# Performance work log

Measured on AMD Instinct MI355X. Metric: run time of the kernel, lower is better.

The kernel has to match this reference:

```python
import jax, jax.numpy as jnp
import numpy as np

N, M, D0, D1, H, E = 1024, 4096, 1024, 512, 512, 64
TAU = 0.5


def setup_inputs() -> dict:
    key = jax.random.key(0)
    ks = jax.random.split(key, 24)
    g = lambda k, shape, s=0.05: (jax.random.normal(k, shape, jnp.float32) * s)
    # 0/1 meta-path neighbor incidence matrices, avg degree ~16
    nei0 = (jax.random.uniform(ks[0], (N, M)) < 0.004).astype(jnp.float32)
    nei1 = (jax.random.uniform(ks[1], (N, M)) < 0.004).astype(jnp.float32)
    def norm_adj(k):
        a = (jax.random.uniform(k, (N, N)) < 0.005).astype(jnp.float32) + jnp.eye(N, dtype=jnp.float32)
        return a / a.sum(1, keepdims=True)
    return dict(
        feat0=g(ks[2], (N, D0), 1.0), feat1=g(ks[3], (M, D1), 1.0), feat2=g(ks[4], (M, D1), 1.0),
        mask_feat=g(ks[5], (N, D0), 1.0),
        nei0=nei0, nei1=nei1,
        adj0=norm_adj(ks[6]), adj1=norm_adj(ks[7]),
        madj0=norm_adj(ks[8]), madj1=norm_adj(ks[9]),
        fc0_w=g(ks[10], (D0, H)), fc0_b=jnp.zeros((H,), jnp.float32),
        fc1_w=g(ks[11], (D1, H)), fc1_b=jnp.zeros((H,), jnp.float32),
        fc2_w=g(ks[12], (D1, H)), fc2_b=jnp.zeros((H,), jnp.float32),
        agg0_w=g(ks[13], (H, H)), agg1_w=g(ks[14], (H, H)),
        gcn_w1=g(ks[15], (H, E)), gcn_b1=jnp.zeros((E,), jnp.float32),
        gcn_w2=g(ks[16], (E, E)), gcn_b2=jnp.zeros((E,), jnp.float32),
        att_w=g(ks[17], (E, E)), att_b=jnp.zeros((E,), jnp.float32),
        att_vec=g(ks[18], (E,)),
        proj_w=g(ks[19], (E, E)), proj_b=jnp.zeros((E,), jnp.float32),
        mlp1_w=g(ks[20], (E, 16)), mlp1_b=jnp.zeros((16,), jnp.float32),
        mlp2_w=g(ks[21], (16, 1)), mlp2_b=jnp.zeros((1,), jnp.float32),
    )


def _l2norm(x):
    # F.normalize(dim=1)
    return x / jnp.maximum(jnp.linalg.norm(x, axis=1, keepdims=True), 1e-12)


def reference(feat0, feat1, feat2, mask_feat, nei0, nei1, adj0, adj1, madj0, madj1,
              fc0_w, fc0_b, fc1_w, fc1_b, fc2_w, fc2_b, agg0_w, agg1_w,
              gcn_w1, gcn_b1, gcn_w2, gcn_b2, att_w, att_b, att_vec,
              proj_w, proj_b, mlp1_w, mlp1_b, mlp2_w, mlp2_b):
    elu = jax.nn.elu
    # aggregate_nei_acm (dropout in eval mode => identity)
    h_tar = elu(feat0 @ fc0_w + fc0_b)                       # [N, H]
    h_mask = elu(mask_feat @ fc0_w + fc0_b)                  # [N, H]
    h_nei = [elu(feat1 @ fc1_w + fc1_b), elu(feat2 @ fc2_w + fc2_b)]  # [M, H]
    neis = [nei0, nei1]
    agg_ws = [agg0_w, agg1_w]
    views, masks = [], []
    for i in range(2):
        cnt = jnp.maximum(neis[i].sum(1, keepdims=True), 1.0)  # nei_index_count, clamped >0
        h_agg = (neis[i] @ h_nei[i]) / cnt                     # sparse neighbor mean, [N, H]
        t = h_agg @ agg_ws[i]
        views.append(elu(h_tar + t))
        masks.append(elu(h_mask + t))

    def gcn(x, adj):
        # 2-layer GCN: relu(A X W1 + b1) -> A H W2 + b2
        h = jax.nn.relu(adj @ (x @ gcn_w1) + gcn_b1)
        return adj @ (h @ gcn_w2) + gcn_b2

    mean_adj = (adj0 + adj1) * 0.5                           # torch.stack(adjs).mean(0)
    z_coarse = gcn(h_tar, mean_adj)                          # [N, E]
    # order: Encoder(view_i, adj_i), Encoder(mask_i, mask_adj_i) per i
    h_fine = [gcn(views[0], adj0), gcn(masks[0], madj0),
              gcn(views[1], adj1), gcn(masks[1], madj1)]
    hs = jnp.stack([_l2norm(h) for h in h_fine])             # [V=4, N, E]
    # semantic attention over views
    e = jnp.einsum('vne,e->v', jnp.tanh(hs @ att_w + att_b), att_vec) / hs.shape[1]
    beta = jax.nn.softmax(e)
    z_fine = jnp.einsum('v,vne->ne', beta, hs)               # [N, E]
    zc = _l2norm(jnp.tanh(z_coarse @ proj_w + proj_b))
    zf = _l2norm(jnp.tanh(z_fine @ proj_w + proj_b))
    # weight_InfoNce
    logits = (zf @ zc.T) / TAU                               # [N, N]
    dots = jnp.exp(logits)
    pair = zf[:, None, :] + zc[None, :, :]                   # [N, N, E] = z_anchor[i] + z[j]
    w = jax.nn.sigmoid(jnp.tanh(pair @ mlp1_w + mlp1_b) @ mlp2_w + mlp2_b)[..., 0]
    denom = jnp.sum(dots * w, axis=1)
    # -log(diag(dots)/denom) = log(denom) - diag(logits)
    loss = jnp.mean(jnp.log(denom) - jnp.diagonal(logits))
    return loss
```

## Files before the change

kernel.cpp:

```cpp
#include <hip/hip_runtime.h>

#define ACT_NONE 0
#define ACT_ELU  1
#define ACT_RELU 2
#define ACT_TANH 3

typedef __attribute__((ext_vector_type(8))) short short8;
typedef __attribute__((ext_vector_type(4))) float f32x4;

__device__ __forceinline__ float frcp(float x) { return __builtin_amdgcn_rcpf(x); }
__device__ __forceinline__ float fexp(float x) { return __expf(x); }
__device__ __forceinline__ float ftanh(float x) {
    return 1.f - 2.f * frcp(fexp(2.f * x) + 1.f);
}
__device__ __forceinline__ float fsigmoid(float x) {
    return frcp(1.f + fexp(-x));
}

__device__ __forceinline__ float apply_act(float v, int act) {
    if (act == ACT_ELU)  return v > 0.f ? v : fexp(v) - 1.f;
    if (act == ACT_RELU) return fmaxf(v, 0.f);
    if (act == ACT_TANH) return ftanh(v);
    return v;
}

__device__ __forceinline__ unsigned short f2bf(float f) {
    unsigned int u = __float_as_uint(f);
    unsigned int r = (u + 0x7fffu + ((u >> 16) & 1u)) >> 16;
    return (unsigned short)r;
}
__device__ __forceinline__ float bf2f(unsigned short u) {
    return __uint_as_float(((unsigned int)u) << 16);
}

__device__ __forceinline__ void xcd_remap(int& bx, int& by, int nx, int ny) {
    if ((ny & 7) == 0) {
        int L = by * nx + bx;
        int xcd = L & 7, j = L >> 3;
        int q = j / nx;
        by = xcd + 8 * q;
        bx = j - q * nx;
    }
}

struct CTDesc { const float* in; unsigned short* out; int R, C, tcols, tile0; };
struct CMDesc { const float* in; unsigned short* out; int start4; };
struct CastArr {
    CTDesc t[8]; int nt; int T;
    CMDesc f[6]; int nf; int total4;
};

__global__ __launch_bounds__(256) void cast_all_kernel(CastArr a) {
    int b = blockIdx.x;
    if (b < a.T) {
        int s = 0;
        while (s + 1 < a.nt && b >= a.t[s + 1].tile0) ++s;
        const CTDesc d = a.t[s];
        int lt = b - d.tile0;
        int tr = lt / d.tcols, tc = lt % d.tcols;
        int r0 = tr * 32, c0 = tc * 32;
        __shared__ float tt[32][33];
        int tx = threadIdx.x & 31, ty = threadIdx.x >> 5;
        for (int i = ty; i < 32; i += 8) {
            int r = r0 + i, c = c0 + tx;
            tt[i][tx] = (r < d.R && c < d.C) ? d.in[(size_t)r * d.C + c] : 0.f;
        }
        __syncthreads();
        for (int i = ty; i < 32; i += 8) {
            int c = c0 + i, r = r0 + tx;
            if (c < d.C && r < d.R) d.out[(size_t)c * d.R + r] = f2bf(tt[tx][i]);
        }
    } else {
        int g4 = (b - a.T) * 256 + threadIdx.x;
        if (g4 >= a.total4) return;
        int s = 0;
        while (s + 1 < a.nf && g4 >= a.f[s + 1].start4) ++s;
        int l4 = g4 - a.f[s].start4;
        float4 v = *reinterpret_cast<const float4*>(a.f[s].in + (size_t)l4 * 4);
        ushort4 o;
        o.x = f2bf(v.x); o.y = f2bf(v.y); o.z = f2bf(v.z); o.w = f2bf(v.w);
        *reinterpret_cast<ushort4*>(a.f[s].out + (size_t)l4 * 4) = o;
    }
}

struct GSeg {
    const unsigned short* A;
    const unsigned short* Bt;
    const unsigned short* Bt2;
    const float* bias;
    const float* bias2;
    float* C;
    unsigned short* Cbf;
    unsigned short* Cbf2;
    int cbf_mlimit;
    int m_split;
    int K;
    int act;
    int mt0;
};
struct GArr { GSeg s[2]; int ns; int N; };

struct KBufs { short8 a0, a1, b0, b1; };

__global__ __launch_bounds__(256) void gemm_seg_kernel(GArr g) {
    int bx = blockIdx.x, by = blockIdx.y;
    xcd_remap(bx, by, gridDim.x, gridDim.y);
    const int mt = by;
    const int si = (g.ns > 1 && mt >= g.s[1].mt0) ? 1 : 0;
    const GSeg s = g.s[si];
    const int K = s.K, N = g.N;
    const int tid = threadIdx.x;
    const int w = tid >> 6, lane = tid & 63;
    const int wr = w >> 1, wc = w & 1;
    const int lr = lane & 15, lk = lane >> 4;
    const int bm = (mt - s.mt0) * 64, bn = bx * 64;
    const unsigned short* Bu = s.Bt;
    const float* bu = s.bias;
    if (bm >= s.m_split) { Bu = s.Bt2; bu = s.bias2; }

    const unsigned short* Ap = s.A + (size_t)(bm + wr * 32 + lr) * K + lk * 8;
    const unsigned short* Bp = Bu + (size_t)(bn + wc * 32 + lr) * K + lk * 8;
    const size_t r16A = (size_t)16 * K;

    f32x4 acc[2][2] = {};
    KBufs u0, u1, u2, u3;
    auto LD = [&](KBufs& u, int kk) {
        kk = kk < K ? kk : 0;
        u.a0 = *reinterpret_cast<const short8*>(Ap + kk);
        u.a1 = *reinterpret_cast<const short8*>(Ap + r16A + kk);
        u.b0 = *reinterpret_cast<const short8*>(Bp + kk);
        u.b1 = *reinterpret_cast<const short8*>(Bp + r16A + kk);
    };
    auto MM = [&](const KBufs& u) {
        acc[0][0] = __builtin_amdgcn_mfma_f32_16x16x32_bf16(u.a0, u.b0, acc[0][0], 0, 0, 0);
        acc[0][1] = __builtin_amdgcn_mfma_f32_16x16x32_bf16(u.a0, u.b1, acc[0][1], 0, 0, 0);
        acc[1][0] = __builtin_amdgcn_mfma_f32_16x16x32_bf16(u.a1, u.b0, acc[1][0], 0, 0, 0);
        acc[1][1] = __builtin_amdgcn_mfma_f32_16x16x32_bf16(u.a1, u.b1, acc[1][1], 0, 0, 0);
    };
    LD(u0, 0); LD(u1, 32); LD(u2, 64);
    for (int k = 0; k < K; k += 128) {
        LD(u3, k + 96);  MM(u0);
        LD(u0, k + 128); MM(u1);
        LD(u1, k + 160); MM(u2);
        LD(u2, k + 192); MM(u3);
    }
    #pragma unroll
    for (int i = 0; i < 2; ++i) {
        #pragma unroll
        for (int j = 0; j < 2; ++j) {
            int gcol = bn + wc * 32 + j * 16 + lr;
            float bv = bu ? bu[gcol] : 0.f;
            #pragma unroll
            for (int r = 0; r < 4; ++r) {
                int grow = bm + wr * 32 + i * 16 + lk * 4 + r;
                float v = apply_act(acc[i][j][r] + bv, s.act);
                if (s.C) s.C[(size_t)grow * N + gcol] = v;
                if (grow < s.cbf_mlimit) {
                    if (s.Cbf)  s.Cbf[(size_t)grow * N + gcol] = f2bf(v);
                } else {
                    if (s.Cbf2) s.Cbf2[(size_t)(grow - s.cbf_mlimit) * N + gcol] = f2bf(v);
                }
            }
        }
    }
}

__global__ __launch_bounds__(256) void gemm_splitk_kernel(
    const unsigned short* __restrict__ A, const unsigned short* __restrict__ Bt,
    const unsigned short* __restrict__ Bt2, int m_split,
    float* __restrict__ C, int M, int K, int N, int ksplit) {
    int bx = blockIdx.x, by = blockIdx.y;
    xcd_remap(bx, by, gridDim.x, gridDim.y);
    const int tid = threadIdx.x;
    const int w = tid >> 6, lane = tid & 63;
    const int wr = w >> 1, wc = w & 1;
    const int lr = lane & 15, lk = lane >> 4;
    const int bm = by * 64, bn = bx * 64;
    const int z = blockIdx.z;
    const int kbeg = z * ksplit;
    const int kend = kbeg + ksplit < K ? kbeg + ksplit : K;
    const int KL = kend - kbeg;
    C += (size_t)z * M * N;
    const unsigned short* Bu = (bm >= m_split) ? Bt2 : Bt;

    const unsigned short* Ap = A + (size_t)(bm + wr * 32 + lr) * K + kbeg + lk * 8;
    const unsigned short* Bp = Bu + (size_t)(bn + wc * 32 + lr) * K + kbeg + lk * 8;
    const size_t r16 = (size_t)16 * K;

    f32x4 acc[2][2] = {};
    KBufs u0, u1, u2, u3;
    auto LD = [&](KBufs& u, int kk) {
        kk = kk < KL ? kk : 0;
        u.a0 = *reinterpret_cast<const short8*>(Ap + kk);
        u.a1 = *reinterpret_cast<const short8*>(Ap + r16 + kk);
        u.b0 = *reinterpret_cast<const short8*>(Bp + kk);
        u.b1 = *reinterpret_cast<const short8*>(Bp + r16 + kk);
    };
    auto MM = [&](const KBufs& u) {
        acc[0][0] = __builtin_amdgcn_mfma_f32_16x16x32_bf16(u.a0, u.b0, acc[0][0], 0, 0, 0);
        acc[0][1] = __builtin_amdgcn_mfma_f32_16x16x32_bf16(u.a0, u.b1, acc[0][1], 0, 0, 0);
        acc[1][0] = __builtin_amdgcn_mfma_f32_16x16x32_bf16(u.a1, u.b0, acc[1][0], 0, 0, 0);
        acc[1][1] = __builtin_amdgcn_mfma_f32_16x16x32_bf16(u.a1, u.b1, acc[1][1], 0, 0, 0);
    };
    LD(u0, 0); LD(u1, 32); LD(u2, 64);
    for (int k = 0; k < KL; k += 128) {
        LD(u3, k + 96);  MM(u0);
        LD(u0, k + 128); MM(u1);
        LD(u1, k + 160); MM(u2);
        LD(u2, k + 192); MM(u3);
    }
    #pragma unroll
    for (int i = 0; i < 2; ++i)
        #pragma unroll
        for (int j = 0; j < 2; ++j) {
            int gcol = bn + wc * 32 + j * 16 + lr;
            #pragma unroll
            for (int r = 0; r < 4; ++r) {
                int grow = bm + wr * 32 + i * 16 + lk * 4 + r;
                C[(size_t)grow * N + gcol] = acc[i][j][r];
            }
        }
}

__global__ __launch_bounds__(256) void neiagg_kernel(
    const float* __restrict__ nei0, const float* __restrict__ nei1,
    const unsigned short* __restrict__ hn0, const unsigned short* __restrict__ hn1,
    unsigned short* __restrict__ hagg) {
    const int row = blockIdx.x, br = blockIdx.y, t = threadIdx.x;
    const float* nei = br ? nei1 : nei0;
    const unsigned short* hn = br ? hn1 : hn0;
    __shared__ int idxs[256];
    __shared__ int cnt;
    if (t == 0) cnt = 0;
    __syncthreads();
    const float4* nr = reinterpret_cast<const float4*>(nei + (size_t)row * 4096);
    for (int j = t; j < 1024; j += 256) {
        float4 v = nr[j];
        if (v.x != 0.f) { int s = atomicAdd(&cnt, 1); if (s < 256) idxs[s] = j * 4 + 0; }
        if (v.y != 0.f) { int s = atomicAdd(&cnt, 1); if (s < 256) idxs[s] = j * 4 + 1; }
        if (v.z != 0.f) { int s = atomicAdd(&cnt, 1); if (s < 256) idxs[s] = j * 4 + 2; }
        if (v.w != 0.f) { int s = atomicAdd(&cnt, 1); if (s < 256) idxs[s] = j * 4 + 3; }
    }
    __syncthreads();
    int n = cnt < 256 ? cnt : 256;
    float inv = frcp(fmaxf((float)cnt, 1.f));
    int c = t * 2;
    float a0 = 0.f, a1 = 0.f, b0 = 0.f, b1 = 0.f;
    int k = 0;
    for (; k + 2 <= n; k += 2) {
        ushort2 u = *reinterpret_cast<const ushort2*>(&hn[(size_t)idxs[k] * 512 + c]);
        ushort2 v = *reinterpret_cast<const ushort2*>(&hn[(size_t)idxs[k + 1] * 512 + c]);
        a0 += bf2f(u.x); a1 += bf2f(u.y);
        b0 += bf2f(v.x); b1 += bf2f(v.y);
    }
    if (k < n) {
        ushort2 u = *reinterpret_cast<const ushort2*>(&hn[(size_t)idxs[k] * 512 + c]);
        a0 += bf2f(u.x); a1 += bf2f(u.y);
    }
    ushort2 o; o.x = f2bf((a0 + b0) * inv); o.y = f2bf((a1 + b1) * inv);
    *reinterpret_cast<ushort2*>(&hagg[((size_t)br * 1024 + row) * 512 + c]) = o;
}

__global__ void addelu_kernel(const unsigned short* __restrict__ ht,
                              const unsigned short* __restrict__ hm,
                              const float* __restrict__ tt, unsigned short* __restrict__ xcat,
                              int nh, int PL) {
    int idx = blockIdx.x * 256 + threadIdx.x;
    if (idx < nh) {
        float h1 = bf2f(ht[idx]), h2 = bf2f(hm[idx]);
        float t0 = tt[idx] + tt[idx + PL];
        float t1 = tt[idx + nh] + tt[idx + nh + PL];
        float a = h1 + t0, b = h2 + t0, c = h1 + t1, d = h2 + t1;
        xcat[(size_t)1 * nh + idx] = f2bf(a > 0.f ? a : fexp(a) - 1.f);
        xcat[(size_t)2 * nh + idx] = f2bf(b > 0.f ? b : fexp(b) - 1.f);
        xcat[(size_t)3 * nh + idx] = f2bf(c > 0.f ? c : fexp(c) - 1.f);
        xcat[(size_t)4 * nh + idx] = f2bf(d > 0.f ? d : fexp(d) - 1.f);
    }
}

__global__ __launch_bounds__(64) void adjprep_kernel(
    const float* __restrict__ adj0, const float* __restrict__ adj1,
    const float* __restrict__ madj0, const float* __restrict__ madj1,
    int* __restrict__ cnts, int* __restrict__ idxs, float* __restrict__ wts) {
    const int row = blockIdx.x, br = blockIdx.y, t = threadIdx.x;
    const float* Aa; const float* Ab = nullptr; float sc = 1.f;
    if (br == 0)      { Aa = adj0; Ab = adj1; sc = 0.5f; }
    else if (br == 1) { Aa = adj0; }
    else if (br == 2) { Aa = madj0; }
    else if (br == 3) { Aa = adj1; }
    else              { Aa = madj1; }
    __shared__ int li[128];
    __shared__ float lw[128];
    __shared__ int cnt;
    if (t == 0) cnt = 0;
    __syncthreads();
    const float4* ar = reinterpret_cast<const float4*>(Aa + (size_t)row * 1024);
    const float4* brp = Ab ? reinterpret_cast<const float4*>(Ab + (size_t)row * 1024) : nullptr;
    for (int j = t; j < 256; j += 64) {
        float4 v = ar[j];
        if (brp) { float4 u = brp[j]; v.x += u.x; v.y += u.y; v.z += u.z; v.w += u.w; }
        if (v.x != 0.f) { int s = atomicAdd(&cnt, 1); if (s < 128) { li[s] = j * 4 + 0; lw[s] = v.x * sc; } }
        if (v.y != 0.f) { int s = atomicAdd(&cnt, 1); if (s < 128) { li[s] = j * 4 + 1; lw[s] = v.y * sc; } }
        if (v.z != 0.f) { int s = atomicAdd(&cnt, 1); if (s < 128) { li[s] = j * 4 + 2; lw[s] = v.z * sc; } }
        if (v.w != 0.f) { int s = atomicAdd(&cnt, 1); if (s < 128) { li[s] = j * 4 + 3; lw[s] = v.w * sc; } }
    }
    __syncthreads();
    int n = cnt < 128 ? cnt : 128;
    size_t base = ((size_t)br * 1024 + row) * 128;
    for (int k = t; k < n; k += 64) { idxs[base + k] = li[k]; wts[base + k] = lw[k]; }
    if (t == 0) cnts[br * 1024 + row] = n;
}

__global__ __launch_bounds__(256) void spmm1_kernel(
    const int* __restrict__ cnts, const int* __restrict__ idxs, const float* __restrict__ wts,
    const float* __restrict__ X, int PL, const float* __restrict__ bias,
    unsigned short* __restrict__ out) {
    const int row = blockIdx.x * 4 + (threadIdx.x >> 6);
    const int br = blockIdx.y, t = threadIdx.x & 63;
    size_t base = ((size_t)br * 1024 + row) * 128;
    int n = cnts[br * 1024 + row];
    const float* Xb = X + (size_t)br * 1024 * 64;
    const float* Xb2 = Xb + PL;
    float acc = bias[t], a1 = 0.f;
    int k = 0;
    for (; k + 2 <= n; k += 2) {
        int   i0 = idxs[base + k], i1 = idxs[base + k + 1];
        float w0 = wts[base + k],  w1 = wts[base + k + 1];
        acc += w0 * (Xb[(size_t)i0 * 64 + t] + Xb2[(size_t)i0 * 64 + t]);
        a1  += w1 * (Xb[(size_t)i1 * 64 + t] + Xb2[(size_t)i1 * 64 + t]);
    }
    if (k < n) {
        int i0 = idxs[base + k];
        acc += wts[base + k] * (Xb[(size_t)i0 * 64 + t] + Xb2[(size_t)i0 * 64 + t]);
    }
    acc += a1;
    out[((size_t)br * 1024 + row) * 64 + t] = f2bf(fmaxf(acc, 0.f));
}

__global__ __launch_bounds__(256) void spmm2_kernel(
    const int* __restrict__ cnts, const int* __restrict__ idxs, const float* __restrict__ wts,
    const unsigned short* __restrict__ H1, const float* __restrict__ w2,
    const float* __restrict__ b2, unsigned short* __restrict__ zcf_bf,
    float* __restrict__ hs, const float* __restrict__ att_w,
    const float* __restrict__ att_b, const float* __restrict__ att_vec,
    float* __restrict__ att_row) {
    const int wv = threadIdx.x >> 6;
    const int row = blockIdx.x * 4 + wv;
    const int br = blockIdx.y, t = threadIdx.x & 63;
    size_t base = ((size_t)br * 1024 + row) * 128;
    int n = cnts[br * 1024 + row];
    const unsigned short* Hb = H1 + (size_t)br * 1024 * 64;
    float g0 = 0.f, g1 = 0.f, g2 = 0.f, g3 = 0.f;
    int k = 0;
    for (; k + 4 <= n; k += 4) {
        g0 += wts[base + k]     * bf2f(Hb[(size_t)idxs[base + k]     * 64 + t]);
        g1 += wts[base + k + 1] * bf2f(Hb[(size_t)idxs[base + k + 1] * 64 + t]);
        g2 += wts[base + k + 2] * bf2f(Hb[(size_t)idxs[base + k + 2] * 64 + t]);
        g3 += wts[base + k + 3] * bf2f(Hb[(size_t)idxs[base + k + 3] * 64 + t]);
    }
    for (; k < n; ++k) g0 += wts[base + k] * bf2f(Hb[(size_t)idxs[base + k] * 64 + t]);
    float g = (g0 + g1) + (g2 + g3);
    __shared__ float rs[4][64];
    rs[wv][t] = g;
    float o = b2[t];
    #pragma unroll
    for (int c = 0; c < 64; ++c) o += rs[wv][c] * w2[c * 64 + t];
    if (br == 0) {
        zcf_bf[(size_t)row * 64 + t] = f2bf(o);
        return;
    }
    float s = o * o;
    #pragma unroll
    for (int q = 32; q; q >>= 1) s += __shfl_down(s, q);
    s = __shfl(s, 0);
    float v = o * frcp(fmaxf(sqrtf(s), 1e-12f));
    hs[((size_t)(br - 1) * 1024 + row) * 64 + t] = v;
    rs[wv][t] = v;
    float sa = att_b[t];
    #pragma unroll
    for (int c = 0; c < 64; ++c) sa += rs[wv][c] * att_w[c * 64 + t];
    float val = ftanh(sa) * att_vec[t];
    #pragma unroll
    for (int q = 32; q; q >>= 1) val += __shfl_down(val, q);
    if (t == 0) att_row[(size_t)(br - 1) * 1024 + row] = val;
}

__global__ __launch_bounds__(256) void attreduce_kernel(const float* __restrict__ att_row,
                                                        float* __restrict__ small) {
    const int v = blockIdx.x, t = threadIdx.x;
    const float* p = att_row + (size_t)v * 1024;
    float s = p[t] + p[t + 256] + p[t + 512] + p[t + 768];
    #pragma unroll
    for (int o = 32; o; o >>= 1) s += __shfl_down(s, o);
    __shared__ float ps[4];
    if ((t & 63) == 0) ps[t >> 6] = s;
    __syncthreads();
    if (t == 0) small[v] = ps[0] + ps[1] + ps[2] + ps[3];
}

__global__ __launch_bounds__(256) void projhead_kernel(
    const unsigned short* __restrict__ zcf_bf, const float* __restrict__ hs,
    const float* __restrict__ small, const float* __restrict__ proj_w,
    const float* __restrict__ proj_b, const float* __restrict__ mlp1_w,
    float* __restrict__ zcat, float* __restrict__ AC1) {
    const int wv = threadIdx.x >> 6;
    const int row = blockIdx.x * 4 + wv;
    const int t = threadIdx.x & 63;
    float zv;
    if (row < 1024) {
        zv = bf2f(zcf_bf[(size_t)row * 64 + t]);
    } else {
        int r = row - 1024;
        float e0 = small[0] * (1.f / 1024.f), e1 = small[1] * (1.f / 1024.f);
        float e2 = small[2] * (1.f / 1024.f), e3 = small[3] * (1.f / 1024.f);
        float mx = fmaxf(fmaxf(e0, e1), fmaxf(e2, e3));
        float x0 = expf(e0 - mx), x1 = expf(e1 - mx), x2 = expf(e2 - mx), x3 = expf(e3 - mx);
        float inv = 1.f / (x0 + x1 + x2 + x3);
        size_t ix = (size_t)r * 64 + t;
        zv = (x0 * hs[ix] + x1 * hs[ix + 65536] +
              x2 * hs[ix + 131072] + x3 * hs[ix + 196608]) * inv;
    }
    __shared__ float rs[4][64];
    rs[wv][t] = zv;
    float p = proj_b[t];
    #pragma unroll
    for (int c = 0; c < 64; ++c) p += rs[wv][c] * proj_w[c * 64 + t];
    p = ftanh(p);
    float s = p * p;
    #pragma unroll
    for (int q = 32; q; q >>= 1) s += __shfl_down(s, q);
    s = __shfl(s, 0);
    float r = p * frcp(fmaxf(sqrtf(s), 1e-12f));
    zcat[(size_t)row * 64 + t] = r;
    rs[wv][t] = r;
    if (t < 16) {
        float a = 0.f;
        #pragma unroll
        for (int c = 0; c < 64; ++c) a += rs[wv][c] * mlp1_w[c * 16 + t];
        AC1[(size_t)row * 16 + t] = a;
    }
}

__global__ __launch_bounds__(256) void infonce_kernel(
    const float* __restrict__ zf, const float* __restrict__ zc,
    const float* __restrict__ A1, const float* __restrict__ C1,
    const float* __restrict__ b1, const float* __restrict__ m2,
    const float* __restrict__ b2v, float* __restrict__ loss_acc) {
    const int i0 = blockIdx.x * 4, t = threadIdx.x;
    __shared__ __align__(16) float zfs[4][64];
    __shared__ float a1b[4][16], m2s[16];
    __shared__ float diag[4];
    __shared__ float wsum[4][4];
    if (t < 64) {
        #pragma unroll
        for (int ii = 0; ii < 4; ++ii) zfs[ii][t] = zf[(size_t)(i0 + ii) * 64 + t];
    }
    if (t < 16) {
        float bb = b1[t];
        #pragma unroll
        for (int ii = 0; ii < 4; ++ii) a1b[ii][t] = A1[(size_t)(i0 + ii) * 16 + t] + bb;
        m2s[t] = m2[t];
    }
    __syncthreads();
    const float b2 = b2v[0];
    float acc[4] = {};
    for (int j = t; j < 1024; j += 256) {
        const float4* zcj = reinterpret_cast<const float4*>(zc + (size_t)j * 64);
        float dot[4] = {};
        #pragma unroll
        for (int e = 0; e < 16; ++e) {
            float4 b = zcj[e];
            #pragma unroll
            for (int ii = 0; ii < 4; ++ii) {
                float4 a = reinterpret_cast<const float4*>(zfs[ii])[e];
                dot[ii] += a.x * b.x + a.y * b.y + a.z * b.z + a.w * b.w;
            }
        }
        float c1j[16];
        #pragma unroll
        for (int q = 0; q < 4; ++q) {
            float4 c4 = reinterpret_cast<const float4*>(C1 + (size_t)j * 16)[q];
            c1j[q * 4 + 0] = c4.x; c1j[q * 4 + 1] = c4.y;
            c1j[q * 4 + 2] = c4.z; c1j[q * 4 + 3] = c4.w;
        }
        #pragma unroll
        for (int ii = 0; ii < 4; ++ii) {
            float logit = dot[ii] * 2.0f;
            float h = b2;
            #pragma unroll
            for (int k = 0; k < 16; ++k) h += ftanh(a1b[ii][k] + c1j[k]) * m2s[k];
            acc[ii] += fexp(logit) * fsigmoid(h);
            if (j == i0 + ii) diag[ii] = logit;
        }
    }
    #pragma unroll
    for (int ii = 0; ii < 4; ++ii) {
        float a = acc[ii];
        #pragma unroll
        for (int o = 32; o; o >>= 1) a += __shfl_down(a, o);
        if ((t & 63) == 0) wsum[t >> 6][ii] = a;
    }
    __syncthreads();
    if (t == 0) {
        float part = 0.f;
        #pragma unroll
        for (int ii = 0; ii < 4; ++ii) {
            float denom = wsum[0][ii] + wsum[1][ii] + wsum[2][ii] + wsum[3][ii];
            part += logf(denom) - diag[ii];
        }
        atomicAdd(loss_acc, part);
    }
}

__global__ void finalize_kernel(const float* __restrict__ small, float* __restrict__ out) {
    if (threadIdx.x == 0) out[0] = small[4] * (1.f / 1024.f);
}

extern "C" void kernel_launch(void* const* d_in, const int* in_sizes, int n_in,
                              void* d_out, int out_size, void* d_ws, size_t ws_size,
                              hipStream_t stream) {
    const float* feat0     = (const float*)d_in[0];
    const float* feat1     = (const float*)d_in[1];
    const float* feat2     = (const float*)d_in[2];
    const float* mask_feat = (const float*)d_in[3];
    const float* nei0      = (const float*)d_in[4];
    const float* nei1      = (const float*)d_in[5];
    const float* adj0      = (const float*)d_in[6];
    const float* adj1      = (const float*)d_in[7];
    const float* madj0     = (const float*)d_in[8];
    const float* madj1     = (const float*)d_in[9];
    const float* fc0_w = (const float*)d_in[10];
    const float* fc0_b = (const float*)d_in[11];
    const float* fc1_w = (const float*)d_in[12];
    const float* fc1_b = (const float*)d_in[13];
    const float* fc2_w = (const float*)d_in[14];
    const float* fc2_b = (const float*)d_in[15];
    const float* agg0_w = (const float*)d_in[16];
    const float* agg1_w = (const float*)d_in[17];
    const float* gcn_w1 = (const float*)d_in[18];
    const float* gcn_b1 = (const float*)d_in[19];
    const float* gcn_w2 = (const float*)d_in[20];
    const float* gcn_b2 = (const float*)d_in[21];
    const float* att_w  = (const float*)d_in[22];
    const float* att_b  = (const float*)d_in[23];
    const float* att_vec = (const float*)d_in[24];
    const float* proj_w = (const float*)d_in[25];
    const float* proj_b = (const float*)d_in[26];
    const float* mlp1_w = (const float*)d_in[27];
    const float* mlp1_b = (const float*)d_in[28];
    const float* mlp2_w = (const float*)d_in[29];
    const float* mlp2_b = (const float*)d_in[30];

    const int N = 1024, M = 4096, D0 = 1024, D1 = 512, H = 512, E = 64;
    typedef unsigned short bf;

    float* W = (float*)d_ws;
    size_t off = 0;
    auto allocf = [&](size_t n) { float* p = W + off; off += n; return p; };
    float* tbuf    = allocf((size_t)2 * 2 * N * H);
    float* xw1cat  = allocf((size_t)2 * 5 * N * E);
    float* hs      = allocf((size_t)4 * N * E);
    float* zcat    = allocf((size_t)2 * N * E);
    float* AC1     = allocf((size_t)2 * N * 16);
    float* att_row = allocf((size_t)4 * N);
    float* small   = allocf(16);
    float* adj_wts = allocf((size_t)5 * 1024 * 128);
    int*   adj_idx = (int*)allocf((size_t)5 * 1024 * 128);
    int*   adj_cnt = (int*)allocf((size_t)5 * 1024);
    bf* BP = (bf*)(W + off);
    size_t boff = 0;
    auto allocb = [&](size_t n) { bf* p = BP + boff; boff += n; return p; };
    bf* feat0_bf = allocb((size_t)N * D0);
    bf* mask_bf  = allocb((size_t)N * D0);
    bf* feat1_bf = allocb((size_t)M * D1);
    bf* feat2_bf = allocb((size_t)M * D1);
    bf* xcat_bf  = allocb((size_t)5 * N * H);
    bf* hmask_bf = allocb((size_t)N * H);
    bf* hnei0_bf = allocb((size_t)M * H);
    bf* hnei1_bf = allocb((size_t)M * H);
    bf* hagg_bf  = allocb((size_t)2 * N * H);
    bf* h1cat_bf = allocb((size_t)5 * N * E);
    bf* zcf_bf   = allocb((size_t)N * E);
    bf* fc0_wT  = allocb((size_t)H * D0);
    bf* fc1_wT  = allocb((size_t)H * D1);
    bf* fc2_wT  = allocb((size_t)H * D1);
    bf* agg0_wT = allocb((size_t)H * H);
    bf* agg1_wT = allocb((size_t)H * H);
    bf* gw1_T   = allocb((size_t)E * H);

    hipMemsetAsync((void*)small, 0, 16 * sizeof(float), stream);

    {
        CastArr a; int tile = 0, i = 0;
        auto addT = [&](const float* in, bf* out, int R, int C) {
            int tc = (C + 31) / 32, trn = (R + 31) / 32;
            a.t[i++] = CTDesc{in, out, R, C, tc, tile};
            tile += tc * trn;
        };
        addT(fc0_w, fc0_wT, D0, H);
        addT(fc1_w, fc1_wT, D1, H);
        addT(fc2_w, fc2_wT, D1, H);
        addT(agg0_w, agg0_wT, H, H);
        addT(agg1_w, agg1_wT, H, H);
        addT(gcn_w1, gw1_T, H, E);
        a.nt = i; a.T = tile;
        int s4 = 0, fi = 0;
        auto addF = [&](const float* in, bf* out, int n) {
            a.f[fi++] = CMDesc{in, out, s4}; s4 += n / 4;
        };
        addF(feat0, feat0_bf, N * D0);
        addF(mask_feat, mask_bf, N * D0);
        addF(feat1, feat1_bf, M * D1);
        addF(feat2, feat2_bf, M * D1);
        a.nf = fi; a.total4 = s4;
        int nb = tile + (s4 + 255) / 256;
        cast_all_kernel<<<nb, 256, 0, stream>>>(a);
    }
    adjprep_kernel<<<dim3(N, 5), 64, 0, stream>>>(adj0, adj1, madj0, madj1,
                                                  adj_cnt, adj_idx, adj_wts);

    {
        GArr g;
        g.s[0] = GSeg{feat0_bf, fc0_wT, nullptr, fc0_b, nullptr,
                      nullptr, xcat_bf, hmask_bf, N, 1 << 30, D0, ACT_ELU, 0};
        g.s[1] = GSeg{feat1_bf, fc1_wT, fc2_wT, fc1_b, fc2_b,
                      nullptr, hnei0_bf, nullptr, 2 * M, M, D1, ACT_ELU, 32};
        g.ns = 2; g.N = H;
        gemm_seg_kernel<<<dim3(H / 64, 32 + 128), 256, 0, stream>>>(g);
    }

    neiagg_kernel<<<dim3(N, 2), 256, 0, stream>>>(nei0, nei1, hnei0_bf, hnei1_bf, hagg_bf);
    gemm_splitk_kernel<<<dim3(H / 64, 2 * N / 64, 2), 256, 0, stream>>>(
        hagg_bf, agg0_wT, agg1_wT, N, tbuf, 2 * N, H, H, 256);
    addelu_kernel<<<(N * H + 255) / 256, 256, 0, stream>>>(xcat_bf, hmask_bf, tbuf, xcat_bf,
                                                           N * H, 2 * N * H);

    gemm_splitk_kernel<<<dim3(1, 5 * N / 64, 2), 256, 0, stream>>>(
        xcat_bf, gw1_T, nullptr, 1 << 30, xw1cat, 5 * N, H, E, 256);
    spmm1_kernel<<<dim3(N / 4, 5), 256, 0, stream>>>(adj_cnt, adj_idx, adj_wts,
                                                     xw1cat, 5 * N * E, gcn_b1, h1cat_bf);
    spmm2_kernel<<<dim3(N / 4, 5), 256, 0, stream>>>(adj_cnt, adj_idx, adj_wts, h1cat_bf,
                                                     gcn_w2, gcn_b2, zcf_bf, hs,
                                                     att_w, att_b, att_vec, att_row);
    attreduce_kernel<<<4, 256, 0, stream>>>(att_row, small);

    projhead_kernel<<<2 * N / 4, 256, 0, stream>>>(zcf_bf, hs, small, proj_w, proj_b,
                                                   mlp1_w, zcat, AC1);

    const float* zc = zcat;
    const float* zf = zcat + (size_t)N * E;
    const float* C1 = AC1;
    const float* A1 = AC1 + (size_t)N * 16;
    infonce_kernel<<<N / 4, 256, 0, stream>>>(zf, zc, A1, C1, mlp1_b, mlp2_w, mlp2_b, small + 4);

    finalize_kernel<<<1, 64, 0, stream>>>(small, (float*)d_out);
}
```

Baseline: 292.3 us.

## Use LDS-staged 128x128 GEMM tiles, fold adjprep into cast kernel, drop atomics

The segmented GEMM now uses 128x128 block tiles and stages A and B through shared memory with global_load_lds, so each wave reuses the staged fragments across a 4x4 MFMA grid instead of loading its own fragments from global memory. The adjacency-to-sparse preprocessing is merged into the cast kernel as extra blocks, which removes one launch. The loss reduction now writes per-block partials and sums them in the finalize kernel, which removes the memset and the atomics. The new GEMM loop syncs twice per 32-wide K step and does not double-buffer, so load latency may be exposed, and the grid has fewer blocks.

Measured after the change: 282.9 us. 1.03x faster.

```diff
diff --git a/kernel.cpp b/kernel.cpp
--- a/kernel.cpp
+++ b/kernel.cpp
@@ -32,6 +32,10 @@
 __device__ __forceinline__ float bf2f(unsigned short u) {
     return __uint_as_float(((unsigned int)u) << 16);
 }
+
+#define GLOAD16(gp, lp) __builtin_amdgcn_global_load_lds( \
+    (const __attribute__((address_space(1))) void*)(gp),  \
+    (__attribute__((address_space(3))) void*)(lp), 16, 0, 0)
 
 __device__ __forceinline__ void xcd_remap(int& bx, int& by, int nx, int ny) {
     if ((ny & 7) == 0) {
@@ -47,11 +51,17 @@
 struct CMDesc { const float* in; unsigned short* out; int start4; };
 struct CastArr {
     CTDesc t[8]; int nt; int T;
-    CMDesc f[6]; int nf; int total4;
+    CMDesc f[6]; int nf; int total4; int F;
+    const float* adj0; const float* adj1; const float* madj0; const float* madj1;
+    int* cnts; int* idxs; float* wts;
 };
 
 __global__ __launch_bounds__(256) void cast_all_kernel(CastArr a) {
     int b = blockIdx.x;
+    __shared__ float tt[32][33];
+    __shared__ int li[4][128];
+    __shared__ float lw[4][128];
+    __shared__ int cnt[4];
     if (b < a.T) {
         int s = 0;
         while (s + 1 < a.nt && b >= a.t[s + 1].tile0) ++s;
@@ -59,7 +69,6 @@
         int lt = b - d.tile0;
         int tr = lt / d.tcols, tc = lt % d.tcols;
         int r0 = tr * 32, c0 = tc * 32;
-        __shared__ float tt[32][33];
         int tx = threadIdx.x & 31, ty = threadIdx.x >> 5;
         for (int i = ty; i < 32; i += 8) {
             int r = r0 + i, c = c0 + tx;
@@ -70,7 +79,7 @@
             int c = c0 + i, r = r0 + tx;
             if (c < d.C && r < d.R) d.out[(size_t)c * d.R + r] = f2bf(tt[tx][i]);
         }
-    } else {
+    } else if (b < a.T + a.F) {
         int g4 = (b - a.T) * 256 + threadIdx.x;
         if (g4 >= a.total4) return;
         int s = 0;
@@ -80,6 +89,31 @@
         ushort4 o;
         o.x = f2bf(v.x); o.y = f2bf(v.y); o.z = f2bf(v.z); o.w = f2bf(v.w);
         *reinterpret_cast<ushort4*>(a.f[s].out + (size_t)l4 * 4) = o;
+    } else {
+        int wv = threadIdx.x >> 6, t = threadIdx.x & 63;
+        int p = (b - a.T - a.F) * 4 + wv;
+        int row = p & 1023, br = p >> 10;
+        const float* Aa; const float* Ab = nullptr; float sc = 1.f;
+        if (br == 0)      { Aa = a.adj0; Ab = a.adj1; sc = 0.5f; }
+        else if (br == 1) { Aa = a.adj0; }
+        else if (br == 2) { Aa = a.madj0; }
+        else if (br == 3) { Aa = a.adj1; }
+        else              { Aa = a.madj1; }
+        if (t == 0) cnt[wv] = 0;
+        const float4* ar = reinterpret_cast<const float4*>(Aa + (size_t)row * 1024);
+        const float4* brp = Ab ? reinterpret_cast<const float4*>(Ab + (size_t)row * 1024) : nullptr;
+        for (int j = t; j < 256; j += 64) {
+            float4 v = ar[j];
+            if (brp) { float4 u = brp[j]; v.x += u.x; v.y += u.y; v.z += u.z; v.w += u.w; }
+            if (v.x != 0.f) { int s = atomicAdd(&cnt[wv], 1); if (s < 128) { li[wv][s] = j * 4 + 0; lw[wv][s] = v.x * sc; } }
+            if (v.y != 0.f) { int s = atomicAdd(&cnt[wv], 1); if (s < 128) { li[wv][s] = j * 4 + 1; lw[wv][s] = v.y * sc; } }
+            if (v.z != 0.f) { int s = atomicAdd(&cnt[wv], 1); if (s < 128) { li[wv][s] = j * 4 + 2; lw[wv][s] = v.z * sc; } }
+            if (v.w != 0.f) { int s = atomicAdd(&cnt[wv], 1); if (s < 128) { li[wv][s] = j * 4 + 3; lw[wv][s] = v.w * sc; } }
+        }
+        int n = cnt[wv] < 128 ? cnt[wv] : 128;
+        size_t base = ((size_t)br * 1024 + row) * 128;
+        for (int k = t; k < n; k += 64) { a.idxs[base + k] = li[wv][k]; a.wts[base + k] = lw[wv][k]; }
+        if (t == 0) a.cnts[br * 1024 + row] = n;
     }
 }
 
@@ -89,7 +123,6 @@
     const unsigned short* Bt2;
     const float* bias;
     const float* bias2;
-    float* C;
     unsigned short* Cbf;
     unsigned short* Cbf2;
     int cbf_mlimit;
@@ -100,9 +133,9 @@
 };
 struct GArr { GSeg s[2]; int ns; int N; };
 
-struct KBufs { short8 a0, a1, b0, b1; };
-
 __global__ __launch_bounds__(256) void gemm_seg_kernel(GArr g) {
+    __shared__ unsigned short As[8 * 512];
+    __shared__ unsigned short Bs[8 * 512];
     int bx = blockIdx.x, by = blockIdx.y;
     xcd_remap(bx, by, gridDim.x, gridDim.y);
     const int mt = by;
@@ -113,48 +146,51 @@
     const int w = tid >> 6, lane = tid & 63;
     const int wr = w >> 1, wc = w & 1;
     const int lr = lane & 15, lk = lane >> 4;
-    const int bm = (mt - s.mt0) * 64, bn = bx * 64;
+    const int bm = (mt - s.mt0) * 128, bn = bx * 128;
     const unsigned short* Bu = s.Bt;
     const float* bu = s.bias;
     if (bm >= s.m_split) { Bu = s.Bt2; bu = s.bias2; }
 
-    const unsigned short* Ap = s.A + (size_t)(bm + wr * 32 + lr) * K + lk * 8;
-    const unsigned short* Bp = Bu + (size_t)(bn + wc * 32 + lr) * K + lk * 8;
-    const size_t r16A = (size_t)16 * K;
-
-    f32x4 acc[2][2] = {};
-    KBufs u0, u1, u2, u3;
-    auto LD = [&](KBufs& u, int kk) {
-        kk = kk < K ? kk : 0;
-        u.a0 = *reinterpret_cast<const short8*>(Ap + kk);
-        u.a1 = *reinterpret_cast<const short8*>(Ap + r16A + kk);
-        u.b0 = *reinterpret_cast<const short8*>(Bp + kk);
-        u.b1 = *reinterpret_cast<const short8*>(Bp + r16A + kk);
-    };
-    auto MM = [&](const KBufs& u) {
-        acc[0][0] = __builtin_amdgcn_mfma_f32_16x16x32_bf16(u.a0, u.b0, acc[0][0], 0, 0, 0);
-        acc[0][1] = __builtin_amdgcn_mfma_f32_16x16x32_bf16(u.a0, u.b1, acc[0][1], 0, 0, 0);
-        acc[1][0] = __builtin_amdgcn_mfma_f32_16x16x32_bf16(u.a1, u.b0, acc[1][0], 0, 0, 0);
-        acc[1][1] = __builtin_amdgcn_mfma_f32_16x16x32_bf16(u.a1, u.b1, acc[1][1], 0, 0, 0);
-    };
-    LD(u0, 0); LD(u1, 32); LD(u2, 64);
-    for (int k = 0; k < K; k += 128) {
-        LD(u3, k + 96);  MM(u0);
-        LD(u0, k + 128); MM(u1);
-        LD(u1, k + 160); MM(u2);
-        LD(u2, k + 192); MM(u3);
-    }
-    #pragma unroll
-    for (int i = 0; i < 2; ++i) {
-        #pragma unroll
-        for (int j = 0; j < 2; ++j) {
-            int gcol = bn + wc * 32 + j * 16 + lr;
+    const unsigned short* ga0 = s.A + (size_t)(bm + (2 * w)     * 16 + lr) * K + lk * 8;
+    const unsigned short* ga1 = s.A + (size_t)(bm + (2 * w + 1) * 16 + lr) * K + lk * 8;
+    const unsigned short* gb0 = Bu  + (size_t)(bn + (2 * w)     * 16 + lr) * K + lk * 8;
+    const unsigned short* gb1 = Bu  + (size_t)(bn + (2 * w + 1) * 16 + lr) * K + lk * 8;
+    unsigned short* la0 = &As[(2 * w) * 512];
+    unsigned short* la1 = &As[(2 * w + 1) * 512];
+    unsigned short* lb0 = &Bs[(2 * w) * 512];
+    unsigned short* lb1 = &Bs[(2 * w + 1) * 512];
+
+    f32x4 acc[4][4] = {};
+    for (int k0 = 0; k0 < K; k0 += 32) {
+        GLOAD16(ga0 + k0, la0);
+        GLOAD16(ga1 + k0, la1);
+        GLOAD16(gb0 + k0, lb0);
+        GLOAD16(gb1 + k0, lb1);
+        __syncthreads();
+        short8 a[4], b[4];
+        #pragma unroll
+        for (int i = 0; i < 4; ++i)
+            a[i] = *reinterpret_cast<const short8*>(&As[(4 * wr + i) * 512 + lane * 8]);
+        #pragma unroll
+        for (int j = 0; j < 4; ++j)
+            b[j] = *reinterpret_cast<const short8*>(&Bs[(4 * wc + j) * 512 + lane * 8]);
+        #pragma unroll
+        for (int i = 0; i < 4; ++i)
+            #pragma unroll
+            for (int j = 0; j < 4; ++j)
+                acc[i][j] = __builtin_amdgcn_mfma_f32_16x16x32_bf16(a[i], b[j], acc[i][j], 0, 0, 0);
+        __syncthreads();
+    }
+    #pragma unroll
+    for (int i = 0; i < 4; ++i) {
+        #pragma unroll
+        for (int j = 0; j < 4; ++j) {
+            int gcol = bn + wc * 64 + j * 16 + lr;
             float bv = bu ? bu[gcol] : 0.f;
             #pragma unroll
             for (int r = 0; r < 4; ++r) {
-                int grow = bm + wr * 32 + i * 16 + lk * 4 + r;
+                int grow = bm + wr * 64 + i * 16 + lk * 4 + r;
                 float v = apply_act(acc[i][j][r] + bv, s.act);
-                if (s.C) s.C[(size_t)grow * N + gcol] = v;
                 if (grow < s.cbf_mlimit) {
                     if (s.Cbf)  s.Cbf[(size_t)grow * N + gcol] = f2bf(v);
                 } else {
@@ -164,6 +200,8 @@
         }
     }
 }
+
+struct KBufs { short8 a0, a1, b0, b1; };
 
 __global__ __launch_bounds__(256) void gemm_splitk_kernel(
     const unsigned short* __restrict__ A, const unsigned short* __restrict__ Bt,
@@ -278,39 +316,6 @@
     }
 }
 
-__global__ __launch_bounds__(64) void adjprep_kernel(
-    const float* __restrict__ adj0, const float* __restrict__ adj1,
-    const float* __restrict__ madj0, const float* __restrict__ madj1,
-    int* __restrict__ cnts, int* __restrict__ idxs, float* __restrict__ wts) {
-    const int row = blockIdx.x, br = blockIdx.y, t = threadIdx.x;
-    const float* Aa; const float* Ab = nullptr; float sc = 1.f;
-    if (br == 0)      { Aa = adj0; Ab = adj1; sc = 0.5f; }
-    else if (br == 1) { Aa = adj0; }
-    else if (br == 2) { Aa = madj0; }
-    else if (br == 3) { Aa = adj1; }
-    else              { Aa = madj1; }
-    __shared__ int li[128];
-    __shared__ float lw[128];
-    __shared__ int cnt;
-    if (t == 0) cnt = 0;
-    __syncthreads();
-    const float4* ar = reinterpret_cast<const float4*>(Aa + (size_t)row * 1024);
-    const float4* brp = Ab ? reinterpret_cast<const float4*>(Ab + (size_t)row * 1024) : nullptr;
-    for (int j = t; j < 256; j += 64) {
-        float4 v = ar[j];
-        if (brp) { float4 u = brp[j]; v.x += u.x; v.y += u.y; v.z += u.z; v.w += u.w; }
-        if (v.x != 0.f) { int s = atomicAdd(&cnt, 1); if (s < 128) { li[s] = j * 4 + 0; lw[s] = v.x * sc; } }
-        if (v.y != 0.f) { int s = atomicAdd(&cnt, 1); if (s < 128) { li[s] = j * 4 + 1; lw[s] = v.y * sc; } }
-        if (v.z != 0.f) { int s = atomicAdd(&cnt, 1); if (s < 128) { li[s] = j * 4 + 2; lw[s] = v.z * sc; } }
-        if (v.w != 0.f) { int s = atomicAdd(&cnt, 1); if (s < 128) { li[s] = j * 4 + 3; lw[s] = v.w * sc; } }
-    }
-    __syncthreads();
-    int n = cnt < 128 ? cnt : 128;
-    size_t base = ((size_t)br * 1024 + row) * 128;
-    for (int k = t; k < n; k += 64) { idxs[base + k] = li[k]; wts[base + k] = lw[k]; }
-    if (t == 0) cnts[br * 1024 + row] = n;
-}
-
 __global__ __launch_bounds__(256) void spmm1_kernel(
     const int* __restrict__ cnts, const int* __restrict__ idxs, const float* __restrict__ wts,
     const float* __restrict__ X, int PL, const float* __restrict__ bias,
@@ -445,7 +450,7 @@
     const float* __restrict__ zf, const float* __restrict__ zc,
     const float* __restrict__ A1, const float* __restrict__ C1,
     const float* __restrict__ b1, const float* __restrict__ m2,
-    const float* __restrict__ b2v, float* __restrict__ loss_acc) {
+    const float* __restrict__ b2v, float* __restrict__ loss_part) {
     const int i0 = blockIdx.x * 4, t = threadIdx.x;
     __shared__ __align__(16) float zfs[4][64];
     __shared__ float a1b[4][16], m2s[16];
@@ -508,12 +513,20 @@
             float denom = wsum[0][ii] + wsum[1][ii] + wsum[2][ii] + wsum[3][ii];
             part += logf(denom) - diag[ii];
         }
-        atomicAdd(loss_acc, part);
-    }
-}
-
-__global__ void finalize_kernel(const float* __restrict__ small, float* __restrict__ out) {
-    if (threadIdx.x == 0) out[0] = small[4] * (1.f / 1024.f);
+        loss_part[blockIdx.x] = part;
+    }
+}
+
+__global__ __launch_bounds__(256) void finalize_kernel(const float* __restrict__ loss_part,
+                                                       float* __restrict__ out) {
+    const int t = threadIdx.x;
+    float s = loss_part[t];
+    #pragma unroll
+    for (int o = 32; o; o >>= 1) s += __shfl_down(s, o);
+    __shared__ float ps[4];
+    if ((t & 63) == 0) ps[t >> 6] = s;
+    __syncthreads();
+    if (t == 0) out[0] = (ps[0] + ps[1] + ps[2] + ps[3]) * (1.f / 1024.f);
 }
 
 extern "C" void kernel_launch(void* const* d_in, const int* in_sizes, int n_in,
@@ -564,6 +577,7 @@
     float* AC1     = allocf((size_t)2 * N * 16);
     float* att_row = allocf((size_t)4 * N);
     float* small   = allocf(16);
+    float* loss_part = allocf(256);
     float* adj_wts = allocf((size_t)5 * 1024 * 128);
     int*   adj_idx = (int*)allocf((size_t)5 * 1024 * 128);
     int*   adj_cnt = (int*)allocf((size_t)5 * 1024);
@@ -588,8 +602,6 @@
     bf* agg1_wT = allocb((size_t)H * H);
     bf* gw1_T   = allocb((size_t)E * H);
 
-    hipMemsetAsync((void*)small, 0, 16 * sizeof(float), stream);
-
     {
         CastArr a; int tile = 0, i = 0;
         auto addT = [&](const float* in, bf* out, int R, int C) {
@@ -612,21 +624,21 @@
         addF(mask_feat, mask_bf, N * D0);
         addF(feat1, feat1_bf, M * D1);
         addF(feat2, feat2_bf, M * D1);
-        a.nf = fi; a.total4 = s4;
-        int nb = tile + (s4 + 255) / 256;
+        a.nf = fi; a.total4 = s4; a.F = (s4 + 255) / 256;
+        a.adj0 = adj0; a.adj1 = adj1; a.madj0 = madj0; a.madj1 = madj1;
+        a.cnts = adj_cnt; a.idxs = adj_idx; a.wts = adj_wts;
+        int nb = a.T + a.F + (5 * 1024) / 4;
         cast_all_kernel<<<nb, 256, 0, stream>>>(a);
     }
-    adjprep_kernel<<<dim3(N, 5), 64, 0, stream>>>(adj0, adj1, madj0, madj1,
-                                                  adj_cnt, adj_idx, adj_wts);
 
     {
         GArr g;
         g.s[0] = GSeg{feat0_bf, fc0_wT, nullptr, fc0_b, nullptr,
-                      nullptr, xcat_bf, hmask_bf, N, 1 << 30, D0, ACT_ELU, 0};
+                      xcat_bf, hmask_bf, N, 1 << 30, D0, ACT_ELU, 0};
         g.s[1] = GSeg{feat1_bf, fc1_wT, fc2_wT, fc1_b, fc2_b,
-                      nullptr, hnei0_bf, nullptr, 2 * M, M, D1, ACT_ELU, 32};
+                      hnei0_bf, nullptr, 2 * M, M, D1, ACT_ELU, 16};
         g.ns = 2; g.N = H;
-        gemm_seg_kernel<<<dim3(H / 64, 32 + 128), 256, 0, stream>>>(g);
+        gemm_seg_kernel<<<dim3(H / 128, 16 + 64), 256, 0, stream>>>(g);
     }
 
     neiagg_kernel<<<dim3(N, 2), 256, 0, stream>>>(nei0, nei1, hnei0_bf, hnei1_bf, hagg_bf);
@@ -651,7 +663,7 @@
     const float* zf = zcat + (size_t)N * E;
     const float* C1 = AC1;
     const float* A1 = AC1 + (size_t)N * 16;
-    infonce_kernel<<<N / 4, 256, 0, stream>>>(zf, zc, A1, C1, mlp1_b, mlp2_w, mlp2_b, small + 4);
-
-    finalize_kernel<<<1, 64, 0, stream>>>(small, (float*)d_out);
-}
+    infonce_kernel<<<N / 4, 256, 0, stream>>>(zf, zc, A1, C1, mlp1_b, mlp2_w, mlp2_b, loss_part);
+
+    finalize_kernel<<<1, 256, 0, stream>>>(loss_part, (float*)d_out);
+}
```
